# Kernel optimization log

Hardware: AMD Instinct MI355X
Metric: run time of the kernel (lower is better)

## Reference

```python
import jax, jax.numpy as jnp
import numpy as np

E = 1024        # embedding_dim
H = 16          # num_heads
DR = 1          # downsample_rate
INT = E // DR   # internal_dim
HD = INT // H   # head dim
B, NQ, NK = 4, 2048, 2048


def setup_inputs() -> dict:
    key = jax.random.key(0)
    ks = jax.random.split(key, 11)
    s_in = 1.0 / np.sqrt(E)
    s_int = 1.0 / np.sqrt(INT)
    return {
        "q": jax.random.normal(ks[0], (B, NQ, E), jnp.float32),
        "k": jax.random.normal(ks[1], (B, NK, E), jnp.float32),
        "v": jax.random.normal(ks[2], (B, NK, E), jnp.float32),
        "wq": jax.random.normal(ks[3], (E, INT), jnp.float32) * s_in,
        "bq": jnp.zeros((INT,), jnp.float32),
        "wk": jax.random.normal(ks[4], (E, INT), jnp.float32) * s_in,
        "bk": jnp.zeros((INT,), jnp.float32),
        "wv": jax.random.normal(ks[5], (E, INT), jnp.float32) * s_in,
        "bv": jnp.zeros((INT,), jnp.float32),
        "wo": jax.random.normal(ks[6], (INT, E), jnp.float32) * s_int,
        "bo": jnp.zeros((E,), jnp.float32),
    }


def _heads(x):
    # (B, N, INT) -> (B, H, N, HD)
    b, n, c = x.shape
    return x.reshape(b, n, H, c // H).transpose(0, 2, 1, 3)


def reference(q, k, v, wq, bq, wk, bk, wv, bv, wo, bo):
    qh = _heads(q @ wq + bq)          # (B,H,NQ,HD)
    kh = _heads(k @ wk + bk)          # (B,H,NK,HD)
    vh = _heads(v @ wv + bv)          # (B,H,NK,HD)
    scale = 1.0 / np.sqrt(HD)
    attn = jnp.einsum('bhqd,bhkd->bhqk', qh, kh) * scale  # (B,H,NQ,NK)
    attn = jax.nn.softmax(attn, axis=-1)
    out = jnp.einsum('bhqk,bhkd->bhqd', attn, vh)          # (B,H,NQ,HD)
    out = out.transpose(0, 2, 1, 3).reshape(q.shape[0], qh.shape[2], INT)
    return out @ wo + bo
```

## Files before the change

### kernel.cpp

```cpp
#include <hip/hip_runtime.h>
#include <hip/hip_bf16.h>
#include <cstdint>
#include <cstddef>

typedef __bf16 bf16_t;
typedef __bf16 bf16x8 __attribute__((ext_vector_type(8)));
typedef float f32x4 __attribute__((ext_vector_type(4)));
typedef float f32x16 __attribute__((ext_vector_type(16)));
typedef uint32_t u32;

#define EDIM 1024
#define HH 16
#define HD 64
#define NSEQ 2048
#define QSCALE 0.18033688011f

__device__ __forceinline__ void async_copy16(const bf16_t* gsrc, bf16_t* lds_dst) {
    __builtin_amdgcn_global_load_lds(
        (const __attribute__((address_space(1))) uint32_t*)gsrc,
        (__attribute__((address_space(3))) uint32_t*)lds_dst,
        16, 0, 0);
}

__device__ __forceinline__ bf16x8 cvt8(float4 x, float4 y) {
    bf16x8 v = {(bf16_t)x.x, (bf16_t)x.y, (bf16_t)x.z, (bf16_t)x.w,
                (bf16_t)y.x, (bf16_t)y.y, (bf16_t)y.z, (bf16_t)y.w};
    return v;
}

__global__ void prep(const float* __restrict__ w0, const float* __restrict__ w1,
                     const float* __restrict__ w2, const float* __restrict__ w3,
                     bf16_t* __restrict__ o0, bf16_t* __restrict__ o1,
                     bf16_t* __restrict__ o2, bf16_t* __restrict__ o3,
                     const float* __restrict__ q, const float* __restrict__ k,
                     const float* __restrict__ v,
                     bf16_t* __restrict__ xq, bf16_t* __restrict__ xk,
                     bf16_t* __restrict__ xv, int do_cvt) {
    __shared__ bf16_t t[64][65];
    const int id = blockIdx.x;
    const int tid = threadIdx.x;
    if (id < 1024) {
        const int z = id >> 8, rem = id & 255, kt = rem >> 4, nt = rem & 15;
        const float* in;
        bf16_t* out;
        switch (z) {
            case 0: in = w0; out = o0; break;
            case 1: in = w1; out = o1; break;
            case 2: in = w2; out = o2; break;
            default: in = w3; out = o3; break;
        }
        #pragma unroll
        for (int i = 0; i < 16; i++) {
            int idx = i * 256 + tid;
            int r = idx >> 6, c = idx & 63;
            t[r][c] = (bf16_t)in[(size_t)(kt * 64 + r) * 1024 + nt * 64 + c];
        }
        __syncthreads();
        #pragma unroll
        for (int i = 0; i < 16; i++) {
            int idx = i * 256 + tid;
            int r = idx >> 6, c = idx & 63;
            out[(size_t)(nt * 64 + r) * 1024 + kt * 64 + c] = t[c][r];
        }
    } else {
        if (!do_cvt) return;
        const int j = id - 1024;
        const int which = j >> 12;
        const int blk = j & 4095;
        const float* in;
        bf16_t* out;
        switch (which) {
            case 0: in = q; out = xq; break;
            case 1: in = k; out = xk; break;
            default: in = v; out = xv; break;
        }
        size_t i = ((size_t)blk * 256 + tid) * 8;
        float4 x = *(const float4*)(in + i);
        float4 y = *(const float4*)(in + i + 4);
        *(bf16x8*)(out + i) = cvt8(x, y);
    }
}

__global__ __launch_bounds__(256, 2)
void gemm_qkv_async(const bf16_t* __restrict__ Xq, const bf16_t* __restrict__ Xk,
                    const bf16_t* __restrict__ Xv,
                    const bf16_t* __restrict__ Wq, const bf16_t* __restrict__ Wk,
                    const bf16_t* __restrict__ Wv,
                    const float* __restrict__ bq, const float* __restrict__ bk,
                    const float* __restrict__ bv,
                    bf16_t* __restrict__ Qh, bf16_t* __restrict__ Kh,
                    bf16_t* __restrict__ Vt) {
    constexpr int BM = 128, BN = 128, BK = 64, K = 1024, NT = K / BK;
    __shared__ bf16_t Asm[2][BM * BK];
    __shared__ bf16_t Bsm[2][BN * BK];
    const int tid = threadIdx.x;
    const int wave = tid >> 6, lane = tid & 63;
    const int quad = lane >> 4, l15 = lane & 15;
    const int bx = blockIdx.x, by = blockIdx.y;
    const int mt = (by >> 3) * 8 + bx;
    const int n0 = (by & 7) * BN;
    const int wt = mt >> 6;
    const int m0 = (mt - wt * 64) * BM;
    const int wm = (wave & 1) * 64, wn = (wave >> 1) * 64;

    const bf16_t* A    = wt == 0 ? Xq : (wt == 1 ? Xk : Xv);
    const bf16_t* Bt   = wt == 0 ? Wq : (wt == 1 ? Wk : Wv);
    const float*  bias = wt == 0 ? bq : (wt == 1 ? bk : bv);
    bf16_t*       Cout = wt == 0 ? Qh : (wt == 1 ? Kh : Vt);
    const float oscale = wt == 0 ? QSCALE : 1.0f;

    f32x4 acc[4][4] = {};

    auto stage = [&](int t, int buf) {
        const int k0 = t * BK;
        #pragma unroll
        for (int i = 0; i < 4; i++) {
            int s = i * 256 + tid;
            int row = s >> 3, kc = (s & 7) ^ (row & 7);
            async_copy16(A + (size_t)(m0 + row) * K + k0 + kc * 8, &Asm[buf][s * 8]);
        }
        #pragma unroll
        for (int i = 0; i < 4; i++) {
            int s = i * 256 + tid;
            int row = s >> 3, kc = (s & 7) ^ (row & 7);
            async_copy16(Bt + (size_t)(n0 + row) * K + k0 + kc * 8, &Bsm[buf][s * 8]);
        }
    };

    stage(0, 0);
    stage(1, 1);
    asm volatile("s_waitcnt vmcnt(8)" ::: "memory");
    __builtin_amdgcn_s_barrier();
    __builtin_amdgcn_sched_barrier(0);

    for (int t = 0; t < NT; ++t) {
        const int buf = t & 1;
        bf16x8 af[2][4], bfr[2][4];
        #pragma unroll
        for (int ks = 0; ks < 2; ks++) {
            #pragma unroll
            for (int mi = 0; mi < 4; mi++) {
                int row = wm + mi * 16 + l15;
                int g = ks * 4 + quad;
                af[ks][mi] = *(const bf16x8*)&Asm[buf][row * BK + ((g ^ (row & 7)) * 8)];
            }
            #pragma unroll
            for (int ni = 0; ni < 4; ni++) {
                int row = wn + ni * 16 + l15;
                int g = ks * 4 + quad;
                bfr[ks][ni] = *(const bf16x8*)&Bsm[buf][row * BK + ((g ^ (row & 7)) * 8)];
            }
        }
        #pragma unroll
        for (int ks = 0; ks < 2; ks++)
            #pragma unroll
            for (int mi = 0; mi < 4; mi++)
                #pragma unroll
                for (int ni = 0; ni < 4; ni++)
                    acc[mi][ni] = __builtin_amdgcn_mfma_f32_16x16x32_bf16(
                        af[ks][mi], bfr[ks][ni], acc[mi][ni], 0, 0, 0);

        if (t + 1 < NT) {
            __builtin_amdgcn_s_barrier();
            __builtin_amdgcn_sched_barrier(0);
            if (t + 2 < NT) {
                stage(t + 2, buf);
                asm volatile("s_waitcnt vmcnt(8)" ::: "memory");
            } else {
                asm volatile("s_waitcnt vmcnt(0)" ::: "memory");
            }
            asm volatile("s_waitcnt lgkmcnt(0)" ::: "memory");
            __builtin_amdgcn_s_barrier();
            __builtin_amdgcn_sched_barrier(0);
        }
    }

    #pragma unroll
    for (int mi = 0; mi < 4; mi++) {
        #pragma unroll
        for (int ni = 0; ni < 4; ni++) {
            #pragma unroll
            for (int r = 0; r < 4; r++) {
                int m = m0 + wm + mi * 16 + quad * 4 + r;
                int nch = n0 + wn + ni * 16 + l15;
                float v = (acc[mi][ni][r] + bias[nch]) * oscale;
                int b = m >> 11, n = m & 2047;
                int h = nch >> 6, d = nch & 63;
                if (wt < 2)
                    Cout[(((size_t)(b * HH + h)) * NSEQ + n) * HD + d] = (bf16_t)v;
                else
                    Cout[(((size_t)(b * HH + h)) * HD + d) * NSEQ + n] = (bf16_t)v;
            }
        }
    }
}

__global__ __launch_bounds__(256, 2)
void gemm_qkv(const float* __restrict__ Aq, const float* __restrict__ Ak,
              const float* __restrict__ Av,
              const bf16_t* __restrict__ Wq, const bf16_t* __restrict__ Wk,
              const bf16_t* __restrict__ Wv,
              const float* __restrict__ bq, const float* __restrict__ bk,
              const float* __restrict__ bv,
              bf16_t* __restrict__ Qh, bf16_t* __restrict__ Kh,
              bf16_t* __restrict__ Vt) {
    constexpr int BM = 128, BN = 128, BK = 64, K = 1024, NT = K / BK;
    __shared__ bf16_t Asm[2][BM * BK];
    __shared__ bf16_t Bsm[2][BN * BK];
    const int tid = threadIdx.x;
    const int wave = tid >> 6, lane = tid & 63;
    const int quad = lane >> 4, l15 = lane & 15;
    const int bx = blockIdx.x, by = blockIdx.y;
    const int mt = (by >> 3) * 8 + bx;
    const int n0 = (by & 7) * BN;
    const int wt = mt >> 6;
    const int m0 = (mt - wt * 64) * BM;
    const int wm = (wave & 1) * 64, wn = (wave >> 1) * 64;

    const float*  A    = wt == 0 ? Aq : (wt == 1 ? Ak : Av);
    const bf16_t* Bt   = wt == 0 ? Wq : (wt == 1 ? Wk : Wv);
    const float*  bias = wt == 0 ? bq : (wt == 1 ? bk : bv);
    bf16_t*       Cout = wt == 0 ? Qh : (wt == 1 ? Kh : Vt);
    const float oscale = wt == 0 ? QSCALE : 1.0f;

    f32x4 acc[4][4] = {};
    float4 ar[8];

    auto loadA = [&](int t) {
        const int k0 = t * BK;
        #pragma unroll
        for (int i = 0; i < 4; i++) {
            int s = i * 256 + tid;
            int row = s >> 3, kc = (s & 7) ^ (row & 7);
            const float* sp = A + (size_t)(m0 + row) * K + k0 + kc * 8;
            ar[2 * i]     = *(const float4*)sp;
            ar[2 * i + 1] = *(const float4*)(sp + 4);
        }
    };
    auto writeA = [&](int buf) {
        #pragma unroll
        for (int i = 0; i < 4; i++) {
            int s = i * 256 + tid;
            *(bf16x8*)&Asm[buf][s * 8] = cvt8(ar[2 * i], ar[2 * i + 1]);
        }
    };
    auto stageB = [&](int t, int buf) {
        const int k0 = t * BK;
        #pragma unroll
        for (int i = 0; i < 4; i++) {
            int s = i * 256 + tid;
            int row = s >> 3, kc = (s & 7) ^ (row & 7);
            async_copy16(Bt + (size_t)(n0 + row) * K + k0 + kc * 8, &Bsm[buf][s * 8]);
        }
    };

    loadA(0);
    stageB(0, 0);
    writeA(0);
    stageB(1, 1);
    asm volatile("s_waitcnt vmcnt(4)" ::: "memory");
    loadA(1);
    asm volatile("s_waitcnt lgkmcnt(0)" ::: "memory");
    __builtin_amdgcn_s_barrier();
    __builtin_amdgcn_sched_barrier(0);

    for (int t = 0; t < NT; ++t) {
        const int buf = t & 1;
        bf16x8 af[2][4], bfr[2][4];
        #pragma unroll
        for (int ks = 0; ks < 2; ks++) {
            #pragma unroll
            for (int mi = 0; mi < 4; mi++) {
                int row = wm + mi * 16 + l15;
                int g = ks * 4 + quad;
                af[ks][mi] = *(const bf16x8*)&Asm[buf][row * BK + ((g ^ (row & 7)) * 8)];
            }
            #pragma unroll
            for (int ni = 0; ni < 4; ni++) {
                int row = wn + ni * 16 + l15;
                int g = ks * 4 + quad;
                bfr[ks][ni] = *(const bf16x8*)&Bsm[buf][row * BK + ((g ^ (row & 7)) * 8)];
            }
        }
        #pragma unroll
        for (int ks = 0; ks < 2; ks++)
            #pragma unroll
            for (int mi = 0; mi < 4; mi++)
                #pragma unroll
                for (int ni = 0; ni < 4; ni++)
                    acc[mi][ni] = __builtin_amdgcn_mfma_f32_16x16x32_bf16(
                        af[ks][mi], bfr[ks][ni], acc[mi][ni], 0, 0, 0);

        if (t + 1 < NT) {
            __builtin_amdgcn_s_barrier();
            __builtin_amdgcn_sched_barrier(0);
            writeA(buf ^ 1);
            if (t + 2 < NT) {
                stageB(t + 2, buf);
                asm volatile("s_waitcnt vmcnt(4)" ::: "memory");
                loadA(t + 2);
            } else {
                asm volatile("s_waitcnt vmcnt(0)" ::: "memory");
            }
            asm volatile("s_waitcnt lgkmcnt(0)" ::: "memory");
            __builtin_amdgcn_s_barrier();
            __builtin_amdgcn_sched_barrier(0);
        }
    }

    #pragma unroll
    for (int mi = 0; mi < 4; mi++) {
        #pragma unroll
        for (int ni = 0; ni < 4; ni++) {
            #pragma unroll
            for (int r = 0; r < 4; r++) {
                int m = m0 + wm + mi * 16 + quad * 4 + r;
                int nch = n0 + wn + ni * 16 + l15;
                float v = (acc[mi][ni][r] + bias[nch]) * oscale;
                int b = m >> 11, n = m & 2047;
                int h = nch >> 6, d = nch & 63;
                if (wt < 2)
                    Cout[(((size_t)(b * HH + h)) * NSEQ + n) * HD + d] = (bf16_t)v;
                else
                    Cout[(((size_t)(b * HH + h)) * HD + d) * NSEQ + n] = (bf16_t)v;
            }
        }
    }
}

__global__ __launch_bounds__(256, 2)
void gemm_out(const bf16_t* __restrict__ A, const bf16_t* __restrict__ Bt,
              const float* __restrict__ bias, float* __restrict__ C) {
    constexpr int BM = 128, BN = 128, BK = 64, K = 1024, N = 1024, NT = K / BK;
    __shared__ bf16_t Asm[2][BM * BK];
    __shared__ bf16_t Bsm[2][BN * BK];
    const int tid = threadIdx.x;
    const int wave = tid >> 6, lane = tid & 63;
    const int quad = lane >> 4, l15 = lane & 15;
    const int bx = blockIdx.x, by = blockIdx.y;
    const int n0 = (by & 7) * BN;
    const int m0 = ((by >> 3) * 8 + bx) * BM;
    const int wm = (wave & 1) * 64, wn = (wave >> 1) * 64;

    f32x4 acc[4][4] = {};

    auto stage = [&](int t, int buf) {
        const int k0 = t * BK;
        #pragma unroll
        for (int i = 0; i < 4; i++) {
            int s = i * 256 + tid;
            int row = s >> 3, kc = (s & 7) ^ (row & 7);
            async_copy16(A + (size_t)(m0 + row) * K + k0 + kc * 8, &Asm[buf][s * 8]);
        }
        #pragma unroll
        for (int i = 0; i < 4; i++) {
            int s = i * 256 + tid;
            int row = s >> 3, kc = (s & 7) ^ (row & 7);
            async_copy16(Bt + (size_t)(n0 + row) * K + k0 + kc * 8, &Bsm[buf][s * 8]);
        }
    };

    stage(0, 0);
    stage(1, 1);
    asm volatile("s_waitcnt vmcnt(8)" ::: "memory");
    __builtin_amdgcn_s_barrier();
    __builtin_amdgcn_sched_barrier(0);

    for (int t = 0; t < NT; ++t) {
        const int buf = t & 1;
        bf16x8 af[2][4], bfr[2][4];
        #pragma unroll
        for (int ks = 0; ks < 2; ks++) {
            #pragma unroll
            for (int mi = 0; mi < 4; mi++) {
                int row = wm + mi * 16 + l15;
                int g = ks * 4 + quad;
                af[ks][mi] = *(const bf16x8*)&Asm[buf][row * BK + ((g ^ (row & 7)) * 8)];
            }
            #pragma unroll
            for (int ni = 0; ni < 4; ni++) {
                int row = wn + ni * 16 + l15;
                int g = ks * 4 + quad;
                bfr[ks][ni] = *(const bf16x8*)&Bsm[buf][row * BK + ((g ^ (row & 7)) * 8)];
            }
        }
        #pragma unroll
        for (int ks = 0; ks < 2; ks++)
            #pragma unroll
            for (int mi = 0; mi < 4; mi++)
                #pragma unroll
                for (int ni = 0; ni < 4; ni++)
                    acc[mi][ni] = __builtin_amdgcn_mfma_f32_16x16x32_bf16(
                        af[ks][mi], bfr[ks][ni], acc[mi][ni], 0, 0, 0);

        if (t + 1 < NT) {
            __builtin_amdgcn_s_barrier();
            __builtin_amdgcn_sched_barrier(0);
            if (t + 2 < NT) {
                stage(t + 2, buf);
                asm volatile("s_waitcnt vmcnt(8)" ::: "memory");
            } else {
                asm volatile("s_waitcnt vmcnt(0)" ::: "memory");
            }
            asm volatile("s_waitcnt lgkmcnt(0)" ::: "memory");
            __builtin_amdgcn_s_barrier();
            __builtin_amdgcn_sched_barrier(0);
        }
    }

    #pragma unroll
    for (int mi = 0; mi < 4; mi++) {
        #pragma unroll
        for (int ni = 0; ni < 4; ni++) {
            #pragma unroll
            for (int r = 0; r < 4; r++) {
                int m = m0 + wm + mi * 16 + quad * 4 + r;
                int nch = n0 + wn + ni * 16 + l15;
                C[(size_t)m * N + nch] = acc[mi][ni][r] + bias[nch];
            }
        }
    }
}

union PW { u32 w[4]; bf16x8 v; };

__device__ __forceinline__ u32 pack_bf16(float lo, float hi) {
    union { bf16_t h[2]; u32 u; } x;
    x.h[0] = (bf16_t)lo;
    x.h[1] = (bf16_t)hi;
    return x.u;
}

__device__ __forceinline__ void half_swap(u32& a, u32& b) {
    auto r = __builtin_amdgcn_permlane32_swap(a, b, false, false);
    a = r[0];
    b = r[1];
}

__device__ __forceinline__ void softmax_pack(const f32x16 sa, float* lp,
                                             PW& f0, PW& f1) {
    float p[16];
    #pragma unroll
    for (int r = 0; r < 16; r++) {
        p[r] = __builtin_amdgcn_exp2f(sa[r]);
        lp[r & 3] += p[r];
    }
    u32 x0 = pack_bf16(p[0],  p[1]),  x1 = pack_bf16(p[2],  p[3]);
    u32 x2 = pack_bf16(p[4],  p[5]),  x3 = pack_bf16(p[6],  p[7]);
    u32 x4 = pack_bf16(p[8],  p[9]),  x5 = pack_bf16(p[10], p[11]);
    u32 x6 = pack_bf16(p[12], p[13]), x7 = pack_bf16(p[14], p[15]);
    half_swap(x0, x2); half_swap(x1, x3);
    half_swap(x4, x6); half_swap(x5, x7);
    f0.w[0] = x0; f0.w[1] = x1; f0.w[2] = x2; f0.w[3] = x3;
    f1.w[0] = x4; f1.w[1] = x5; f1.w[2] = x6; f1.w[3] = x7;
}

__global__ __launch_bounds__(256, 4)
void attn_kernel(const bf16_t* __restrict__ Qh, const bf16_t* __restrict__ Kh,
                 const bf16_t* __restrict__ Vt, bf16_t* __restrict__ out) {
    __shared__ bf16_t Ks[2][64 * 64];
    __shared__ bf16_t Vs[2][64 * 64];
    const int tid = threadIdx.x, wave = tid >> 6, lane = tid & 63;
    const int l31 = lane & 31, hi = lane >> 5;
    const int B = blockIdx.x;
    const int qt = (B >> 3) & 15;
    const int bh = (B >> 7) * 8 + (B & 7);
    const int b = bh >> 4, h = bh & 15;

    const bf16_t* kbase = Kh + (size_t)bh * NSEQ * HD;
    const bf16_t* vbase = Vt + (size_t)bh * HD * NSEQ;

    bf16x8 qf[4];
    {
        const bf16_t* qrow =
            Qh + ((size_t)bh * NSEQ + qt * 128 + wave * 32 + l31) * HD + hi * 8;
        #pragma unroll
        for (int s = 0; s < 4; s++) qf[s] = *(const bf16x8*)(qrow + s * 16);
    }

    const bf16_t *ks0, *ks1, *vs0, *vs1;
    {
        int r0 = tid >> 3, c0 = tid & 7;
        int s1 = tid + 256;
        int r1 = s1 >> 3, c1 = s1 & 7;
        ks0 = kbase + r0 * HD + (c0 ^ (r0 & 7)) * 8;
        ks1 = kbase + r1 * HD + (c1 ^ (r1 & 7)) * 8;
        vs0 = vbase + (size_t)r0 * NSEQ + (c0 ^ (r0 & 7)) * 8;
        vs1 = vbase + (size_t)r1 * NSEQ + (c1 ^ (r1 & 7)) * 8;
    }

    async_copy16(ks0, &Ks[0][tid * 8]);
    async_copy16(ks1, &Ks[0][(tid + 256) * 8]);
    async_copy16(vs0, &Vs[0][tid * 8]);
    async_copy16(vs1, &Vs[0][(tid + 256) * 8]);

    f32x16 oacc[2] = {};
    float lp[4] = {};

    for (int t = 0; t < 32; t++) {
        const int cur = t & 1;
        __syncthreads();

        if (t < 31) {
            ks0 += 64 * HD; ks1 += 64 * HD;
            vs0 += 64;      vs1 += 64;
            async_copy16(ks0, &Ks[cur ^ 1][tid * 8]);
            async_copy16(ks1, &Ks[cur ^ 1][(tid + 256) * 8]);
            async_copy16(vs0, &Vs[cur ^ 1][tid * 8]);
            async_copy16(vs1, &Vs[cur ^ 1][(tid + 256) * 8]);
        }

        const f32x16 zero = {};
        f32x16 sacc0, sacc1;
        {
            int g = hi;
            int row0 = l31, row1 = 32 + l31;
            bf16x8 ak0 = *(const bf16x8*)&Ks[cur][row0 * 64 + ((g ^ (row0 & 7)) * 8)];
            bf16x8 ak1 = *(const bf16x8*)&Ks[cur][row1 * 64 + ((g ^ (row1 & 7)) * 8)];
            __builtin_amdgcn_s_setprio(1);
            sacc0 = __builtin_amdgcn_mfma_f32_32x32x16_bf16(ak0, qf[0], zero, 0, 0, 0);
            sacc1 = __builtin_amdgcn_mfma_f32_32x32x16_bf16(ak1, qf[0], zero, 0, 0, 0);
            __builtin_amdgcn_s_setprio(0);
        }
        #pragma unroll
        for (int s = 1; s < 4; s++) {
            int g = s * 2 + hi;
            int row0 = l31;
            int row1 = 32 + l31;
            bf16x8 ak0 = *(const bf16x8*)&Ks[cur][row0 * 64 + ((g ^ (row0 & 7)) * 8)];
            bf16x8 ak1 = *(const bf16x8*)&Ks[cur][row1 * 64 + ((g ^ (row1 & 7)) * 8)];
            __builtin_amdgcn_s_setprio(1);
            sacc0 = __builtin_amdgcn_mfma_f32_32x32x16_bf16(ak0, qf[s], sacc0, 0, 0, 0);
            sacc1 = __builtin_amdgcn_mfma_f32_32x32x16_bf16(ak1, qf[s], sacc1, 0, 0, 0);
            __builtin_amdgcn_s_setprio(0);
        }

        PW pa[4];
        softmax_pack(sacc0, lp, pa[0], pa[1]);
        softmax_pack(sacc1, lp, pa[2], pa[3]);

        #pragma unroll
        for (int dt = 0; dt < 2; dt++) {
            #pragma unroll
            for (int ks = 0; ks < 4; ks++) {
                int row = dt * 32 + l31;
                int g = ks * 2 + hi;
                bf16x8 bv = *(const bf16x8*)&Vs[cur][row * 64 + ((g ^ (row & 7)) * 8)];
                __builtin_amdgcn_s_setprio(1);
                oacc[dt] = __builtin_amdgcn_mfma_f32_32x32x16_bf16(
                    pa[ks].v, bv, oacc[dt], 0, 0, 0);
                __builtin_amdgcn_s_setprio(0);
            }
        }
    }

    float lsum = (lp[0] + lp[1]) + (lp[2] + lp[3]);
    lsum += __shfl_xor(lsum, 32, 64);
    float linv = 1.f / lsum;
    float rinv[16];
    #pragma unroll
    for (int r = 0; r < 16; r++) {
        int q = (r & 3) + 8 * (r >> 2) + 4 * hi;
        rinv[r] = __shfl(linv, q, 64);
    }

    const int n0 = qt * 128 + wave * 32;
    #pragma unroll
    for (int dt = 0; dt < 2; dt++) {
        int c = h * 64 + dt * 32 + l31;
        #pragma unroll
        for (int r = 0; r < 16; r++) {
            int q = (r & 3) + 8 * (r >> 2) + 4 * hi;
            out[((size_t)b * NSEQ + n0 + q) * EDIM + c] = (bf16_t)(oacc[dt][r] * rinv[r]);
        }
    }
}

extern "C" void kernel_launch(void* const* d_in, const int* in_sizes, int n_in,
                              void* d_out, int out_size, void* d_ws, size_t ws_size,
                              hipStream_t stream) {
    const float* q  = (const float*)d_in[0];
    const float* k  = (const float*)d_in[1];
    const float* v  = (const float*)d_in[2];
    const float* wq = (const float*)d_in[3];
    const float* bq = (const float*)d_in[4];
    const float* wk = (const float*)d_in[5];
    const float* bk = (const float*)d_in[6];
    const float* wv = (const float*)d_in[7];
    const float* bv = (const float*)d_in[8];
    const float* wo = (const float*)d_in[9];
    const float* bo = (const float*)d_in[10];
    float* out = (float*)d_out;

    char* ws = (char*)d_ws;
    bf16_t* wqt = (bf16_t*)(ws + ((size_t)0  << 20));
    bf16_t* wkt = (bf16_t*)(ws + ((size_t)2  << 20));
    bf16_t* wvt = (bf16_t*)(ws + ((size_t)4  << 20));
    bf16_t* wot = (bf16_t*)(ws + ((size_t)6  << 20));

    bf16_t* Qh  = (bf16_t*)(ws + ((size_t)8  << 20));
    bf16_t* Kh  = (bf16_t*)(ws + ((size_t)24 << 20));
    bf16_t* Vt  = (bf16_t*)(ws + ((size_t)40 << 20));
    bf16_t* ao  = (bf16_t*)(ws + ((size_t)56 << 20));
    bf16_t* Xq  = (bf16_t*)(ws + ((size_t)72 << 20));
    bf16_t* Xk  = (bf16_t*)(ws + ((size_t)88 << 20));
    bf16_t* Xv  = (bf16_t*)(ws + ((size_t)104 << 20));

    const bool big = ws_size >= ((size_t)120 << 20);

    prep<<<dim3(13312), dim3(256), 0, stream>>>(wq, wk, wv, wo, wqt, wkt, wvt, wot,
                                                q, k, v, Xq, Xk, Xv, big ? 1 : 0);

    if (big) {
        gemm_qkv_async<<<dim3(8, 192), dim3(256), 0, stream>>>(Xq, Xk, Xv,
                                                               wqt, wkt, wvt,
                                                               bq, bk, bv, Qh, Kh, Vt);
    } else {
        gemm_qkv<<<dim3(8, 192), dim3(256), 0, stream>>>(q, k, v, wqt, wkt, wvt,
                                                         bq, bk, bv, Qh, Kh, Vt);
    }

    attn_kernel<<<1024, dim3(256), 0, stream>>>(Qh, Kh, Vt, ao);

    gemm_out<<<dim3(8, 64), dim3(256), 0, stream>>>(ao, wot, bo, out);
}
```

Baseline: 331.9 us.

## Process two 32-row query tiles per wave in attention kernel to reuse K/V

Each wave now handles 64 query rows (two 32-row sub-tiles) instead of 32, so every K and V fragment loaded from LDS feeds twice as many MFMAs. The grid drops from 1024 to 512 blocks and launch bounds go from 4 to 2 blocks per SM to make room for the doubled accumulators and Q fragments. This halves global K/V traffic per query and the LDS reads per MFMA, at the cost of higher register pressure and fewer blocks (512 for 256 CUs), which can hurt occupancy and load balance.

```diff
diff --git a/kernel.cpp b/kernel.cpp
--- a/kernel.cpp
+++ b/kernel.cpp
@@ -455,7 +455,7 @@
     f1.w[0] = x4; f1.w[1] = x5; f1.w[2] = x6; f1.w[3] = x7;
 }
 
-__global__ __launch_bounds__(256, 4)
+__global__ __launch_bounds__(256, 2)
 void attn_kernel(const bf16_t* __restrict__ Qh, const bf16_t* __restrict__ Kh,
                  const bf16_t* __restrict__ Vt, bf16_t* __restrict__ out) {
     __shared__ bf16_t Ks[2][64 * 64];
@@ -463,19 +463,23 @@
     const int tid = threadIdx.x, wave = tid >> 6, lane = tid & 63;
     const int l31 = lane & 31, hi = lane >> 5;
     const int B = blockIdx.x;
-    const int qt = (B >> 3) & 15;
-    const int bh = (B >> 7) * 8 + (B & 7);
+    const int qt = (B >> 3) & 7;
+    const int bh = (B >> 6) * 8 + (B & 7);
     const int b = bh >> 4, h = bh & 15;
 
     const bf16_t* kbase = Kh + (size_t)bh * NSEQ * HD;
     const bf16_t* vbase = Vt + (size_t)bh * HD * NSEQ;
 
-    bf16x8 qf[4];
+    bf16x8 qfA[4], qfB[4];
     {
-        const bf16_t* qrow =
-            Qh + ((size_t)bh * NSEQ + qt * 128 + wave * 32 + l31) * HD + hi * 8;
-        #pragma unroll
-        for (int s = 0; s < 4; s++) qf[s] = *(const bf16x8*)(qrow + s * 16);
+        const bf16_t* qrowA =
+            Qh + ((size_t)bh * NSEQ + qt * 256 + wave * 64 + l31) * HD + hi * 8;
+        const bf16_t* qrowB = qrowA + 32 * HD;
+        #pragma unroll
+        for (int s = 0; s < 4; s++) {
+            qfA[s] = *(const bf16x8*)(qrowA + s * 16);
+            qfB[s] = *(const bf16x8*)(qrowB + s * 16);
+        }
     }
 
     const bf16_t *ks0, *ks1, *vs0, *vs1;
@@ -494,8 +498,8 @@
     async_copy16(vs0, &Vs[0][tid * 8]);
     async_copy16(vs1, &Vs[0][(tid + 256) * 8]);
 
-    f32x16 oacc[2] = {};
-    float lp[4] = {};
+    f32x16 oaccA[2] = {}, oaccB[2] = {};
+    float lpA[4] = {}, lpB[4] = {};
 
     for (int t = 0; t < 32; t++) {
         const int cur = t & 1;
@@ -511,15 +515,17 @@
         }
 
         const f32x16 zero = {};
-        f32x16 sacc0, sacc1;
+        f32x16 s0A, s1A, s0B, s1B;
         {
             int g = hi;
             int row0 = l31, row1 = 32 + l31;
             bf16x8 ak0 = *(const bf16x8*)&Ks[cur][row0 * 64 + ((g ^ (row0 & 7)) * 8)];
             bf16x8 ak1 = *(const bf16x8*)&Ks[cur][row1 * 64 + ((g ^ (row1 & 7)) * 8)];
             __builtin_amdgcn_s_setprio(1);
-            sacc0 = __builtin_amdgcn_mfma_f32_32x32x16_bf16(ak0, qf[0], zero, 0, 0, 0);
-            sacc1 = __builtin_amdgcn_mfma_f32_32x32x16_bf16(ak1, qf[0], zero, 0, 0, 0);
+            s0A = __builtin_amdgcn_mfma_f32_32x32x16_bf16(ak0, qfA[0], zero, 0, 0, 0);
+            s1A = __builtin_amdgcn_mfma_f32_32x32x16_bf16(ak1, qfA[0], zero, 0, 0, 0);
+            s0B = __builtin_amdgcn_mfma_f32_32x32x16_bf16(ak0, qfB[0], zero, 0, 0, 0);
+            s1B = __builtin_amdgcn_mfma_f32_32x32x16_bf16(ak1, qfB[0], zero, 0, 0, 0);
             __builtin_amdgcn_s_setprio(0);
         }
         #pragma unroll
@@ -530,14 +536,18 @@
             bf16x8 ak0 = *(const bf16x8*)&Ks[cur][row0 * 64 + ((g ^ (row0 & 7)) * 8)];
             bf16x8 ak1 = *(const bf16x8*)&Ks[cur][row1 * 64 + ((g ^ (row1 & 7)) * 8)];
             __builtin_amdgcn_s_setprio(1);
-            sacc0 = __builtin_amdgcn_mfma_f32_32x32x16_bf16(ak0, qf[s], sacc0, 0, 0, 0);
-            sacc1 = __builtin_amdgcn_mfma_f32_32x32x16_bf16(ak1, qf[s], sacc1, 0, 0, 0);
+            s0A = __builtin_amdgcn_mfma_f32_32x32x16_bf16(ak0, qfA[s], s0A, 0, 0, 0);
+            s1A = __builtin_amdgcn_mfma_f32_32x32x16_bf16(ak1, qfA[s], s1A, 0, 0, 0);
+            s0B = __builtin_amdgcn_mfma_f32_32x32x16_bf16(ak0, qfB[s], s0B, 0, 0, 0);
+            s1B = __builtin_amdgcn_mfma_f32_32x32x16_bf16(ak1, qfB[s], s1B, 0, 0, 0);
             __builtin_amdgcn_s_setprio(0);
         }
 
-        PW pa[4];
-        softmax_pack(sacc0, lp, pa[0], pa[1]);
-        softmax_pack(sacc1, lp, pa[2], pa[3]);
+        PW paA[4], paB[4];
+        softmax_pack(s0A, lpA, paA[0], paA[1]);
+        softmax_pack(s1A, lpA, paA[2], paA[3]);
+        softmax_pack(s0B, lpB, paB[0], paB[1]);
+        softmax_pack(s1B, lpB, paB[2], paB[3]);
 
         #pragma unroll
         for (int dt = 0; dt < 2; dt++) {
@@ -547,31 +557,56 @@
                 int g = ks * 2 + hi;
                 bf16x8 bv = *(const bf16x8*)&Vs[cur][row * 64 + ((g ^ (row & 7)) * 8)];
                 __builtin_amdgcn_s_setprio(1);
-                oacc[dt] = __builtin_amdgcn_mfma_f32_32x32x16_bf16(
-                    pa[ks].v, bv, oacc[dt], 0, 0, 0);
+                oaccA[dt] = __builtin_amdgcn_mfma_f32_32x32x16_bf16(
+                    paA[ks].v, bv, oaccA[dt], 0, 0, 0);
+                oaccB[dt] = __builtin_amdgcn_mfma_f32_32x32x16_bf16(
+                    paB[ks].v, bv, oaccB[dt], 0, 0, 0);
                 __builtin_amdgcn_s_setprio(0);
             }
         }
     }
 
-    float lsum = (lp[0] + lp[1]) + (lp[2] + lp[3]);
-    lsum += __shfl_xor(lsum, 32, 64);
-    float linv = 1.f / lsum;
-    float rinv[16];
-    #pragma unroll
-    for (int r = 0; r < 16; r++) {
-        int q = (r & 3) + 8 * (r >> 2) + 4 * hi;
-        rinv[r] = __shfl(linv, q, 64);
-    }
-
-    const int n0 = qt * 128 + wave * 32;
-    #pragma unroll
-    for (int dt = 0; dt < 2; dt++) {
-        int c = h * 64 + dt * 32 + l31;
+    const int n0 = qt * 256 + wave * 64;
+    {
+        float lsum = (lpA[0] + lpA[1]) + (lpA[2] + lpA[3]);
+        lsum += __shfl_xor(lsum, 32, 64);
+        float linv = 1.f / lsum;
+        float rinv[16];
         #pragma unroll
         for (int r = 0; r < 16; r++) {
             int q = (r & 3) + 8 * (r >> 2) + 4 * hi;
-            out[((size_t)b * NSEQ + n0 + q) * EDIM + c] = (bf16_t)(oacc[dt][r] * rinv[r]);
+            rinv[r] = __shfl(linv, q, 64);
+        }
+        #pragma unroll
+        for (int dt = 0; dt < 2; dt++) {
+            int c = h * 64 + dt * 32 + l31;
+            #pragma unroll
+            for (int r = 0; r < 16; r++) {
+                int q = (r & 3) + 8 * (r >> 2) + 4 * hi;
+                out[((size_t)b * NSEQ + n0 + q) * EDIM + c] =
+                    (bf16_t)(oaccA[dt][r] * rinv[r]);
+            }
+        }
+    }
+    {
+        float lsum = (lpB[0] + lpB[1]) + (lpB[2] + lpB[3]);
+        lsum += __shfl_xor(lsum, 32, 64);
+        float linv = 1.f / lsum;
+        float rinv[16];
+        #pragma unroll
+        for (int r = 0; r < 16; r++) {
+            int q = (r & 3) + 8 * (r >> 2) + 4 * hi;
+            rinv[r] = __shfl(linv, q, 64);
+        }
+        #pragma unroll
+        for (int dt = 0; dt < 2; dt++) {
+            int c = h * 64 + dt * 32 + l31;
+            #pragma unroll
+            for (int r = 0; r < 16; r++) {
+                int q = (r & 3) + 8 * (r >> 2) + 4 * hi;
+                out[((size_t)b * NSEQ + n0 + 32 + q) * EDIM + c] =
+                    (bf16_t)(oaccB[dt][r] * rinv[r]);
+            }
         }
     }
 }
@@ -620,7 +655,7 @@
                                                          bq, bk, bv, Qh, Kh, Vt);
     }
 
-    attn_kernel<<<1024, dim3(256), 0, stream>>>(Qh, Kh, Vt, ao);
+    attn_kernel<<<512, dim3(256), 0, stream>>>(Qh, Kh, Vt, ao);
 
     gemm_out<<<dim3(8, 64), dim3(256), 0, stream>>>(ao, wot, bo, out);
 }
```

After: 328.9 us. About the same (-0.9%).
